# Kernel optimization log

Hardware: AMD Instinct MI355X
Metric: run time of the kernel (lower is better)

## Reference

```python
import math
import jax, jax.numpy as jnp
import numpy as np

DIM = 128
NUM_PROJ = 256
B, H, SEQ = 2, 16, 4096


def _make_orthogonal_S(key):
    # Mirrors QJLWithOrthogonal.__init__: raw Gaussian, QR-orthogonalize each
    # dim-row chunk, scale by sqrt(dim).
    raw = jax.random.normal(key, (NUM_PROJ, DIM), dtype=jnp.float32)
    blocks = []
    for start in range(0, NUM_PROJ, DIM):
        block = raw[start:min(start + DIM, NUM_PROJ)]
        if block.shape[0] <= block.shape[1]:
            q, _ = jnp.linalg.qr(block.T)  # reduced QR of [dim, rows]
            blocks.append(q.T * np.float32(math.sqrt(DIM)))
        else:
            blocks.append(block)
    return jnp.concatenate(blocks, axis=0)[:NUM_PROJ]


def setup_inputs() -> dict:
    key = jax.random.key(0)
    kq, kk, ks = jax.random.split(key, 3)
    query = jax.random.normal(kq, (B, H, SEQ, DIM), dtype=jnp.float32)
    key_t = jax.random.normal(kk, (B, H, SEQ, DIM), dtype=jnp.float32)
    S = _make_orthogonal_S(ks)
    return {"query": query, "key": key_t, "S": S}


def reference(query, key, S):
    # quantize(key): sign of JL projection -> {-1, +1}, shape [B,H,S,m]
    z = jnp.sign(jnp.einsum('bhsd,md->bhsm', key, S))
    # estimate_inner_product(query, z): asymmetric estimator
    qp = jnp.einsum('bhsd,md->bhsm', query, S)
    scale = np.float32(math.sqrt(math.pi / 2) / NUM_PROJ)
    return scale * jnp.sum(qp * z, axis=-1)  # [B,H,S]
```

## Files before the change

### kernel.cpp

```cpp
#include <hip/hip_runtime.h>
#include <hip/hip_bf16.h>


#define DIM        128
#define NPROJ      256
#define TILE_T     32
#define NWG        4096
#define LDS_STRIDE 136
#define TAU        6.0e-3f
#define SCALE      0.0048957583489668f

typedef __attribute__((ext_vector_type(8))) short short8;
typedef __attribute__((ext_vector_type(4))) float f32x4;

static __device__ __forceinline__ unsigned short bf16_rne(float x){
    unsigned int u = __builtin_bit_cast(unsigned int, x);
    u += 0x7FFFu + ((u >> 16) & 1u);
    return (unsigned short)(u >> 16);
}

static __device__ __attribute__((noinline))
float ref_sign(const float* __restrict__ Kg, const float* __restrict__ S,
               int tok, int m){
    const float* kr = Kg + (size_t)tok * DIM;
    const float* sr = S  + (size_t)m   * DIM;
    float acc = 0.f;
#pragma unroll 8
    for (int d = 0; d < DIM; ++d)
        acc = __builtin_fmaf(kr[d], sr[d], acc);
    return (acc > 0.f) ? 1.f : ((acc < 0.f) ? -1.f : 0.f);
}

__global__ void prep_s_kernel(const float* __restrict__ S,
                              unsigned short* __restrict__ shi,
                              unsigned short* __restrict__ slo){
    int t    = blockIdx.x * 256 + threadIdx.x;
    int lane = t & 63;
    int ms   = (t >> 6) & 3;
    int ks   = (t >> 8) & 3;
    int g    = (t >> 10) & 3;
    int m    = g*64 + ms*16 + (lane & 15);
    int d    = ks*32 + (lane >> 4)*8;
    const float4* p = (const float4*)(S + (size_t)m*DIM + d);
    float4 x0 = p[0], x1 = p[1];
    float xs[8] = {x0.x,x0.y,x0.z,x0.w, x1.x,x1.y,x1.z,x1.w};
    size_t base = ((size_t)t) * 8;
    unsigned long long h0=0,h1=0,l0=0,l1=0;
#pragma unroll
    for (int e = 0; e < 4; ++e){
        unsigned short hb = bf16_rne(xs[e]);
        float hf = __builtin_bit_cast(float, (unsigned int)hb << 16);
        h0 |= (unsigned long long)hb                    << (16*e);
        l0 |= (unsigned long long)bf16_rne(xs[e] - hf)  << (16*e);
    }
#pragma unroll
    for (int e = 0; e < 4; ++e){
        unsigned short hb = bf16_rne(xs[4+e]);
        float hf = __builtin_bit_cast(float, (unsigned int)hb << 16);
        h1 |= (unsigned long long)hb                      << (16*e);
        l1 |= (unsigned long long)bf16_rne(xs[4+e] - hf)  << (16*e);
    }
    *(unsigned long long*)(shi + base)     = h0;
    *(unsigned long long*)(shi + base + 4) = h1;
    *(unsigned long long*)(slo + base)     = l0;
    *(unsigned long long*)(slo + base + 4) = l1;
}

template<bool USE_TAB>
static __device__ __forceinline__
void load_afrags(const unsigned short* __restrict__ shi_tab,
                 const unsigned short* __restrict__ slo_tab,
                 const float* __restrict__ S,
                 int wave, int ks, int l16, int quad, int lane,
                 short8 ah[4], short8 al[4], bool need_lo){
    if (USE_TAB){
#pragma unroll
        for (int ms = 0; ms < 4; ++ms){
            size_t off = ((size_t)((wave*4 + ks)*4 + ms)*64 + lane)*8;
            ah[ms] = *(const short8*)(shi_tab + off);
            if (need_lo) al[ms] = *(const short8*)(slo_tab + off);
        }
    } else {
#pragma unroll
        for (int ms = 0; ms < 4; ++ms){
            const float4* p = (const float4*)(S + (size_t)(wave*64 + ms*16 + l16)*DIM
                                              + ks*32 + quad*8);
            float4 x0 = p[0], x1 = p[1];
            float xs[8] = {x0.x,x0.y,x0.z,x0.w, x1.x,x1.y,x1.z,x1.w};
            short8 h, l;
#pragma unroll
            for (int e = 0; e < 8; ++e){
                unsigned short hb = bf16_rne(xs[e]);
                float hf = __builtin_bit_cast(float, (unsigned int)hb << 16);
                h[e] = (short)hb;
                l[e] = (short)bf16_rne(xs[e] - hf);
            }
            ah[ms] = h;
            if (need_lo) al[ms] = l;
        }
    }
}

template<bool USE_TAB>
__global__ __launch_bounds__(256, 4)
void qjl_kernel(const float* __restrict__ Qg, const float* __restrict__ Kg,
                const float* __restrict__ S,
                const unsigned short* __restrict__ shi_tab,
                const unsigned short* __restrict__ slo_tab,
                float* __restrict__ out)
{
    __shared__ unsigned short khi[TILE_T * LDS_STRIDE];
    __shared__ unsigned short klo[TILE_T * LDS_STRIDE];
    __shared__ unsigned short qhi[TILE_T * LDS_STRIDE];
    __shared__ float red[4][TILE_T];

    const int tid  = threadIdx.x;
    const int wave = tid >> 6;
    const int lane = tid & 63;
    const int l16  = lane & 15;
    const int quad = lane >> 4;
    const int tok0 = blockIdx.x * TILE_T;

    {
        const float4* ksrc = (const float4*)(Kg + (size_t)tok0 * DIM);
        const float4* qsrc = (const float4*)(Qg + (size_t)tok0 * DIM);
        float4 kv[4], qv[4];
#pragma unroll
        for (int j = 0; j < 4; ++j){ kv[j] = ksrc[tid + j*256]; qv[j] = qsrc[tid + j*256]; }
#pragma unroll
        for (int j = 0; j < 4; ++j){
            int i   = tid + j*256;
            int row = i >> 5;
            int c   = i & 31;
            float kx[4] = {kv[j].x, kv[j].y, kv[j].z, kv[j].w};
            float qx[4] = {qv[j].x, qv[j].y, qv[j].z, qv[j].w};
            unsigned long long hp = 0, lp = 0, qp = 0;
#pragma unroll
            for (int e = 0; e < 4; ++e){
                unsigned short hb = bf16_rne(kx[e]);
                float hf = __builtin_bit_cast(float, (unsigned int)hb << 16);
                hp |= (unsigned long long)hb                   << (16*e);
                lp |= (unsigned long long)bf16_rne(kx[e] - hf) << (16*e);
                qp |= (unsigned long long)bf16_rne(qx[e])      << (16*e);
            }
            int base = row * LDS_STRIDE + c*4;
            *(unsigned long long*)(khi + base) = hp;
            *(unsigned long long*)(klo + base) = lp;
            *(unsigned long long*)(qhi + base) = qp;
        }
    }
    __syncthreads();

    unsigned int negw = 0, zerow = 0;
    {
        f32x4 accC[4][2];
#pragma unroll
        for (int ms = 0; ms < 4; ++ms)
#pragma unroll
            for (int ts = 0; ts < 2; ++ts)
                accC[ms][ts] = (f32x4){0.f,0.f,0.f,0.f};

#pragma unroll
        for (int ks = 0; ks < 4; ++ks){
            short8 ah[4], al[4];
            load_afrags<USE_TAB>(shi_tab, slo_tab, S, wave, ks, l16, quad, lane,
                                 ah, al, true);
#pragma unroll
            for (int ts = 0; ts < 2; ++ts){
                const int off = (ts*16 + l16) * LDS_STRIDE + ks*32 + quad*8;
                short8 bk = *(const short8*)(khi + off);
                short8 bl = *(const short8*)(klo + off);
#pragma unroll
                for (int ms = 0; ms < 4; ++ms){
                    accC[ms][ts] = __builtin_amdgcn_mfma_f32_16x16x32_bf16(ah[ms], bk, accC[ms][ts], 0,0,0);
                    accC[ms][ts] = __builtin_amdgcn_mfma_f32_16x16x32_bf16(al[ms], bk, accC[ms][ts], 0,0,0);
                    accC[ms][ts] = __builtin_amdgcn_mfma_f32_16x16x32_bf16(ah[ms], bl, accC[ms][ts], 0,0,0);
                }
            }
        }
#pragma unroll
        for (int ts = 0; ts < 2; ++ts){
#pragma unroll
            for (int ms = 0; ms < 4; ++ms){
#pragma unroll
                for (int r = 0; r < 4; ++r){
                    float c = accC[ms][ts][r];
                    float s = (c >= 0.f) ? 1.f : -1.f;
                    if (__builtin_fabsf(c) < TAU)
                        s = ref_sign(Kg, S, tok0 + ts*16 + l16,
                                     wave*64 + ms*16 + quad*4 + r);
                    int bit = (ts*4 + ms)*4 + r;
                    if (s < 0.f)  negw  |= (1u << bit);
                    if (s == 0.f) zerow |= (1u << bit);
                }
            }
        }
    }

    float part0 = 0.f, part1 = 0.f;
    {
        f32x4 accQ[4][2];
#pragma unroll
        for (int ms = 0; ms < 4; ++ms)
#pragma unroll
            for (int ts = 0; ts < 2; ++ts)
                accQ[ms][ts] = (f32x4){0.f,0.f,0.f,0.f};

#pragma unroll
        for (int ks = 0; ks < 4; ++ks){
            short8 ah[4], al_unused[4];
            load_afrags<USE_TAB>(shi_tab, slo_tab, S, wave, ks, l16, quad, lane,
                                 ah, al_unused, false);
#pragma unroll
            for (int ts = 0; ts < 2; ++ts){
                const int off = (ts*16 + l16) * LDS_STRIDE + ks*32 + quad*8;
                short8 bq = *(const short8*)(qhi + off);
#pragma unroll
                for (int ms = 0; ms < 4; ++ms)
                    accQ[ms][ts] = __builtin_amdgcn_mfma_f32_16x16x32_bf16(ah[ms], bq, accQ[ms][ts], 0,0,0);
            }
        }
#pragma unroll
        for (int ts = 0; ts < 2; ++ts){
#pragma unroll
            for (int ms = 0; ms < 4; ++ms){
#pragma unroll
                for (int r = 0; r < 4; ++r){
                    float qp = accQ[ms][ts][r];
                    int bit = (ts*4 + ms)*4 + r;
                    float sv = (zerow >> bit) & 1u ? 0.f
                             : ((negw >> bit) & 1u ? -qp : qp);
                    if (ts) part1 += sv; else part0 += sv;
                }
            }
        }
    }

    part0 += __shfl_xor(part0, 16, 64);
    part0 += __shfl_xor(part0, 32, 64);
    part1 += __shfl_xor(part1, 16, 64);
    part1 += __shfl_xor(part1, 32, 64);
    if (quad == 0){
        red[wave][l16]      = part0;
        red[wave][16 + l16] = part1;
    }
    __syncthreads();
    if (tid < TILE_T)
        out[tok0 + tid] = SCALE * (red[0][tid] + red[1][tid] + red[2][tid] + red[3][tid]);
}

extern "C" void kernel_launch(void* const* d_in, const int* in_sizes, int n_in,
                              void* d_out, int out_size, void* d_ws, size_t ws_size,
                              hipStream_t stream){
    const float* Qg = (const float*)d_in[0];
    const float* Kg = (const float*)d_in[1];
    const float* S  = (const float*)d_in[2];
    float* out = (float*)d_out;

    const size_t tab_elems = (size_t)NPROJ * DIM;
    const size_t need = 2 * tab_elems * sizeof(unsigned short);

    if (d_ws && ws_size >= need){
        unsigned short* shi = (unsigned short*)d_ws;
        unsigned short* slo = shi + tab_elems;
        prep_s_kernel<<<16, 256, 0, stream>>>(S, shi, slo);
        qjl_kernel<true><<<NWG, 256, 0, stream>>>(Qg, Kg, S, shi, slo, out);
    } else {
        qjl_kernel<false><<<NWG, 256, 0, stream>>>(Qg, Kg, S, nullptr, nullptr, out);
    }
}
```

Baseline: 205.5 us.

## Keep S fragments in registers across passes and inline fallback sign check

Loads the high-part S fragments once into registers and reuses them for both the key and query MFMA passes, instead of reloading them per pass. The high-part table loads are issued before the K/Q conversion to overlap global latency. The MFMA loops are restructured per token subtile. The ambiguous-sign fallback now runs as a bitmask loop over only the flagged entries, and the FP32 reference dot product is inlined and vectorised. Occupancy is lowered from 4 to 3 waves per SIMD to make room for the larger register footprint, which risks less latency hiding.

Measured after the change: 263.0 us. +28.0%, slower.

```diff
diff --git a/kernel.cpp b/kernel.cpp
--- a/kernel.cpp
+++ b/kernel.cpp
@@ -19,15 +19,20 @@
     return (unsigned short)(u >> 16);
 }
 
-static __device__ __attribute__((noinline))
+static __device__ __forceinline__
 float ref_sign(const float* __restrict__ Kg, const float* __restrict__ S,
                int tok, int m){
-    const float* kr = Kg + (size_t)tok * DIM;
-    const float* sr = S  + (size_t)m   * DIM;
+    const float4* kr = (const float4*)(Kg + (size_t)tok * DIM);
+    const float4* sr = (const float4*)(S  + (size_t)m   * DIM);
     float acc = 0.f;
-#pragma unroll 8
-    for (int d = 0; d < DIM; ++d)
-        acc = __builtin_fmaf(kr[d], sr[d], acc);
+#pragma unroll
+    for (int i = 0; i < DIM/4; ++i){
+        float4 a = kr[i], b = sr[i];
+        acc = __builtin_fmaf(a.x, b.x, acc);
+        acc = __builtin_fmaf(a.y, b.y, acc);
+        acc = __builtin_fmaf(a.z, b.z, acc);
+        acc = __builtin_fmaf(a.w, b.w, acc);
+    }
     return (acc > 0.f) ? 1.f : ((acc < 0.f) ? -1.f : 0.f);
 }
 
@@ -67,42 +72,7 @@
 }
 
 template<bool USE_TAB>
-static __device__ __forceinline__
-void load_afrags(const unsigned short* __restrict__ shi_tab,
-                 const unsigned short* __restrict__ slo_tab,
-                 const float* __restrict__ S,
-                 int wave, int ks, int l16, int quad, int lane,
-                 short8 ah[4], short8 al[4], bool need_lo){
-    if (USE_TAB){
-#pragma unroll
-        for (int ms = 0; ms < 4; ++ms){
-            size_t off = ((size_t)((wave*4 + ks)*4 + ms)*64 + lane)*8;
-            ah[ms] = *(const short8*)(shi_tab + off);
-            if (need_lo) al[ms] = *(const short8*)(slo_tab + off);
-        }
-    } else {
-#pragma unroll
-        for (int ms = 0; ms < 4; ++ms){
-            const float4* p = (const float4*)(S + (size_t)(wave*64 + ms*16 + l16)*DIM
-                                              + ks*32 + quad*8);
-            float4 x0 = p[0], x1 = p[1];
-            float xs[8] = {x0.x,x0.y,x0.z,x0.w, x1.x,x1.y,x1.z,x1.w};
-            short8 h, l;
-#pragma unroll
-            for (int e = 0; e < 8; ++e){
-                unsigned short hb = bf16_rne(xs[e]);
-                float hf = __builtin_bit_cast(float, (unsigned int)hb << 16);
-                h[e] = (short)hb;
-                l[e] = (short)bf16_rne(xs[e] - hf);
-            }
-            ah[ms] = h;
-            if (need_lo) al[ms] = l;
-        }
-    }
-}
-
-template<bool USE_TAB>
-__global__ __launch_bounds__(256, 4)
+__global__ __launch_bounds__(256, 3)
 void qjl_kernel(const float* __restrict__ Qg, const float* __restrict__ Kg,
                 const float* __restrict__ S,
                 const unsigned short* __restrict__ shi_tab,
@@ -121,117 +91,160 @@
     const int quad = lane >> 4;
     const int tok0 = blockIdx.x * TILE_T;
 
-    {
-        const float4* ksrc = (const float4*)(Kg + (size_t)tok0 * DIM);
-        const float4* qsrc = (const float4*)(Qg + (size_t)tok0 * DIM);
-        float4 kv[4], qv[4];
-#pragma unroll
-        for (int j = 0; j < 4; ++j){ kv[j] = ksrc[tid + j*256]; qv[j] = qsrc[tid + j*256]; }
-#pragma unroll
-        for (int j = 0; j < 4; ++j){
-            int i   = tid + j*256;
-            int row = i >> 5;
-            int c   = i & 31;
-            float kx[4] = {kv[j].x, kv[j].y, kv[j].z, kv[j].w};
-            float qx[4] = {qv[j].x, qv[j].y, qv[j].z, qv[j].w};
-            unsigned long long hp = 0, lp = 0, qp = 0;
-#pragma unroll
-            for (int e = 0; e < 4; ++e){
-                unsigned short hb = bf16_rne(kx[e]);
-                float hf = __builtin_bit_cast(float, (unsigned int)hb << 16);
-                hp |= (unsigned long long)hb                   << (16*e);
-                lp |= (unsigned long long)bf16_rne(kx[e] - hf) << (16*e);
-                qp |= (unsigned long long)bf16_rne(qx[e])      << (16*e);
-            }
-            int base = row * LDS_STRIDE + c*4;
-            *(unsigned long long*)(khi + base) = hp;
-            *(unsigned long long*)(klo + base) = lp;
-            *(unsigned long long*)(qhi + base) = qp;
-        }
+    const float4* ksrc = (const float4*)(Kg + (size_t)tok0 * DIM);
+    const float4* qsrc = (const float4*)(Qg + (size_t)tok0 * DIM);
+    float4 kv[4], qv[4];
+#pragma unroll
+    for (int j = 0; j < 4; ++j){ kv[j] = ksrc[tid + j*256]; qv[j] = qsrc[tid + j*256]; }
+
+    short8 a_hi[4][4];
+    if (USE_TAB){
+#pragma unroll
+        for (int ks = 0; ks < 4; ++ks)
+#pragma unroll
+            for (int ms = 0; ms < 4; ++ms)
+                a_hi[ks][ms] = *(const short8*)(shi_tab +
+                    ((size_t)((wave*4 + ks)*4 + ms)*64 + lane)*8);
+    } else {
+#pragma unroll
+        for (int ks = 0; ks < 4; ++ks)
+#pragma unroll
+            for (int ms = 0; ms < 4; ++ms){
+                const float4* p = (const float4*)(S + (size_t)(wave*64 + ms*16 + l16)*DIM
+                                                  + ks*32 + quad*8);
+                float4 x0 = p[0], x1 = p[1];
+                float xs[8] = {x0.x,x0.y,x0.z,x0.w, x1.x,x1.y,x1.z,x1.w};
+                short8 h;
+#pragma unroll
+                for (int e = 0; e < 8; ++e) h[e] = (short)bf16_rne(xs[e]);
+                a_hi[ks][ms] = h;
+            }
+    }
+
+#pragma unroll
+    for (int j = 0; j < 4; ++j){
+        int i   = tid + j*256;
+        int row = i >> 5;
+        int c   = i & 31;
+        float kx[4] = {kv[j].x, kv[j].y, kv[j].z, kv[j].w};
+        float qx[4] = {qv[j].x, qv[j].y, qv[j].z, qv[j].w};
+        unsigned long long hp = 0, lp = 0, qp = 0;
+#pragma unroll
+        for (int e = 0; e < 4; ++e){
+            unsigned short hb = bf16_rne(kx[e]);
+            float hf = __builtin_bit_cast(float, (unsigned int)hb << 16);
+            hp |= (unsigned long long)hb                   << (16*e);
+            lp |= (unsigned long long)bf16_rne(kx[e] - hf) << (16*e);
+            qp |= (unsigned long long)bf16_rne(qx[e])      << (16*e);
+        }
+        int base = row * LDS_STRIDE + c*4;
+        *(unsigned long long*)(khi + base) = hp;
+        *(unsigned long long*)(klo + base) = lp;
+        *(unsigned long long*)(qhi + base) = qp;
     }
     __syncthreads();
 
+    short8 a_lo[4][4];
+    if (USE_TAB){
+#pragma unroll
+        for (int ks = 0; ks < 4; ++ks)
+#pragma unroll
+            for (int ms = 0; ms < 4; ++ms)
+                a_lo[ks][ms] = *(const short8*)(slo_tab +
+                    ((size_t)((wave*4 + ks)*4 + ms)*64 + lane)*8);
+    } else {
+#pragma unroll
+        for (int ks = 0; ks < 4; ++ks)
+#pragma unroll
+            for (int ms = 0; ms < 4; ++ms){
+                const float4* p = (const float4*)(S + (size_t)(wave*64 + ms*16 + l16)*DIM
+                                                  + ks*32 + quad*8);
+                float4 x0 = p[0], x1 = p[1];
+                float xs[8] = {x0.x,x0.y,x0.z,x0.w, x1.x,x1.y,x1.z,x1.w};
+                short8 l;
+#pragma unroll
+                for (int e = 0; e < 8; ++e){
+                    unsigned short hb = bf16_rne(xs[e]);
+                    float hf = __builtin_bit_cast(float, (unsigned int)hb << 16);
+                    l[e] = (short)bf16_rne(xs[e] - hf);
+                }
+                a_lo[ks][ms] = l;
+            }
+    }
+
     unsigned int negw = 0, zerow = 0;
-    {
-        f32x4 accC[4][2];
-#pragma unroll
-        for (int ms = 0; ms < 4; ++ms)
-#pragma unroll
-            for (int ts = 0; ts < 2; ++ts)
-                accC[ms][ts] = (f32x4){0.f,0.f,0.f,0.f};
+#pragma unroll
+    for (int ts = 0; ts < 2; ++ts){
+        f32x4 accC[4];
+#pragma unroll
+        for (int ms = 0; ms < 4; ++ms) accC[ms] = (f32x4){0.f,0.f,0.f,0.f};
 
 #pragma unroll
         for (int ks = 0; ks < 4; ++ks){
-            short8 ah[4], al[4];
-            load_afrags<USE_TAB>(shi_tab, slo_tab, S, wave, ks, l16, quad, lane,
-                                 ah, al, true);
-#pragma unroll
-            for (int ts = 0; ts < 2; ++ts){
-                const int off = (ts*16 + l16) * LDS_STRIDE + ks*32 + quad*8;
-                short8 bk = *(const short8*)(khi + off);
-                short8 bl = *(const short8*)(klo + off);
-#pragma unroll
-                for (int ms = 0; ms < 4; ++ms){
-                    accC[ms][ts] = __builtin_amdgcn_mfma_f32_16x16x32_bf16(ah[ms], bk, accC[ms][ts], 0,0,0);
-                    accC[ms][ts] = __builtin_amdgcn_mfma_f32_16x16x32_bf16(al[ms], bk, accC[ms][ts], 0,0,0);
-                    accC[ms][ts] = __builtin_amdgcn_mfma_f32_16x16x32_bf16(ah[ms], bl, accC[ms][ts], 0,0,0);
-                }
-            }
-        }
-#pragma unroll
-        for (int ts = 0; ts < 2; ++ts){
+            const int off = (ts*16 + l16) * LDS_STRIDE + ks*32 + quad*8;
+            short8 bk = *(const short8*)(khi + off);
+            short8 bl = *(const short8*)(klo + off);
 #pragma unroll
             for (int ms = 0; ms < 4; ++ms){
-#pragma unroll
-                for (int r = 0; r < 4; ++r){
-                    float c = accC[ms][ts][r];
-                    float s = (c >= 0.f) ? 1.f : -1.f;
-                    if (__builtin_fabsf(c) < TAU)
-                        s = ref_sign(Kg, S, tok0 + ts*16 + l16,
-                                     wave*64 + ms*16 + quad*4 + r);
-                    int bit = (ts*4 + ms)*4 + r;
-                    if (s < 0.f)  negw  |= (1u << bit);
-                    if (s == 0.f) zerow |= (1u << bit);
-                }
-            }
+                accC[ms] = __builtin_amdgcn_mfma_f32_16x16x32_bf16(a_hi[ks][ms], bk, accC[ms], 0,0,0);
+                accC[ms] = __builtin_amdgcn_mfma_f32_16x16x32_bf16(a_hi[ks][ms], bl, accC[ms], 0,0,0);
+            }
+        }
+#pragma unroll
+        for (int ks = 0; ks < 4; ++ks){
+            const int off = (ts*16 + l16) * LDS_STRIDE + ks*32 + quad*8;
+            short8 bk = *(const short8*)(khi + off);
+#pragma unroll
+            for (int ms = 0; ms < 4; ++ms)
+                accC[ms] = __builtin_amdgcn_mfma_f32_16x16x32_bf16(a_lo[ks][ms], bk, accC[ms], 0,0,0);
+        }
+
+        unsigned int ambw = 0;
+#pragma unroll
+        for (int ms = 0; ms < 4; ++ms){
+#pragma unroll
+            for (int r = 0; r < 4; ++r){
+                float c = accC[ms][r];
+                int bit = ms*4 + r;
+                if (c < 0.f) negw |= (1u << (ts*16 + bit));
+                if (__builtin_fabsf(c) < TAU) ambw |= (1u << bit);
+            }
+        }
+        while (ambw){
+            int b = __builtin_ctz(ambw);
+            ambw &= ambw - 1;
+            int ms = (b >> 2) & 3, r = b & 3;
+            float s = ref_sign(Kg, S, tok0 + ts*16 + l16,
+                               wave*64 + ms*16 + quad*4 + r);
+            unsigned int gb = 1u << (ts*16 + b);
+            if (s < 0.f) negw |= gb; else negw &= ~gb;
+            if (s == 0.f) zerow |= gb;
         }
     }
 
     float part0 = 0.f, part1 = 0.f;
-    {
-        f32x4 accQ[4][2];
-#pragma unroll
-        for (int ms = 0; ms < 4; ++ms)
-#pragma unroll
-            for (int ts = 0; ts < 2; ++ts)
-                accQ[ms][ts] = (f32x4){0.f,0.f,0.f,0.f};
-
+#pragma unroll
+    for (int ts = 0; ts < 2; ++ts){
+        f32x4 accQ[4];
+#pragma unroll
+        for (int ms = 0; ms < 4; ++ms) accQ[ms] = (f32x4){0.f,0.f,0.f,0.f};
 #pragma unroll
         for (int ks = 0; ks < 4; ++ks){
-            short8 ah[4], al_unused[4];
-            load_afrags<USE_TAB>(shi_tab, slo_tab, S, wave, ks, l16, quad, lane,
-                                 ah, al_unused, false);
-#pragma unroll
-            for (int ts = 0; ts < 2; ++ts){
-                const int off = (ts*16 + l16) * LDS_STRIDE + ks*32 + quad*8;
-                short8 bq = *(const short8*)(qhi + off);
-#pragma unroll
-                for (int ms = 0; ms < 4; ++ms)
-                    accQ[ms][ts] = __builtin_amdgcn_mfma_f32_16x16x32_bf16(ah[ms], bq, accQ[ms][ts], 0,0,0);
-            }
-        }
-#pragma unroll
-        for (int ts = 0; ts < 2; ++ts){
-#pragma unroll
-            for (int ms = 0; ms < 4; ++ms){
-#pragma unroll
-                for (int r = 0; r < 4; ++r){
-                    float qp = accQ[ms][ts][r];
-                    int bit = (ts*4 + ms)*4 + r;
-                    float sv = (zerow >> bit) & 1u ? 0.f
-                             : ((negw >> bit) & 1u ? -qp : qp);
-                    if (ts) part1 += sv; else part0 += sv;
-                }
+            const int off = (ts*16 + l16) * LDS_STRIDE + ks*32 + quad*8;
+            short8 bq = *(const short8*)(qhi + off);
+#pragma unroll
+            for (int ms = 0; ms < 4; ++ms)
+                accQ[ms] = __builtin_amdgcn_mfma_f32_16x16x32_bf16(a_hi[ks][ms], bq, accQ[ms], 0,0,0);
+        }
+#pragma unroll
+        for (int ms = 0; ms < 4; ++ms){
+#pragma unroll
+            for (int r = 0; r < 4; ++r){
+                float qp = accQ[ms][r];
+                unsigned int gb = ts*16 + ms*4 + r;
+                float sv = (zerow >> gb) & 1u ? 0.f
+                         : ((negw >> gb) & 1u ? -qp : qp);
+                if (ts) part1 += sv; else part0 += sv;
             }
         }
     }
```
